# Optimization experiments

Measured on AMD Instinct MI355X. Metric: run time of the kernel, lower is better.

The kernel has to match this reference:

```python
import jax, jax.numpy as jnp
import numpy as np

N, F, H, C = 4096, 512, 8, 128
LEAKY_ALPHA = 0.2
MASK_VAL = -10e9  # spektral uses -10e9 * (1 - A)


def setup_inputs() -> dict:
    key = jax.random.key(0)
    k1, k2, k3, k4, k5 = jax.random.split(key, 5)
    X = jax.random.normal(k1, (N, F), dtype=jnp.float32)
    # sparse-ish binary adjacency with self loops (dense layout as the layer expects)
    A = (jax.random.uniform(k2, (N, N)) < 0.01).astype(jnp.float32)
    A = jnp.maximum(A, jnp.eye(N, dtype=jnp.float32))
    W = jax.random.normal(k3, (H, F, C), dtype=jnp.float32) * (1.0 / np.sqrt(F))
    a_self = jax.random.normal(k4, (H, C), dtype=jnp.float32) * (1.0 / np.sqrt(C))
    a_neigh = jax.random.normal(k5, (H, C), dtype=jnp.float32) * (1.0 / np.sqrt(C))
    bias = jnp.zeros((H, C), dtype=jnp.float32)
    return {"X": X, "A": A, "W": W, "a_self": a_self, "a_neigh": a_neigh, "bias": bias}


def reference(X, A, W, a_self, a_neigh, bias):
    # per-head feature projection: [H, N, C]
    feats = jnp.einsum("nf,hfc->hnc", X, W)
    # attention scores e_ij = LeakyReLU(a_self . h_i + a_neigh . h_j)
    s_self = jnp.einsum("hnc,hc->hn", feats, a_self)    # [H, N]
    s_neigh = jnp.einsum("hnc,hc->hn", feats, a_neigh)  # [H, N]
    dense = s_self[:, :, None] + s_neigh[:, None, :]    # [H, N, N]
    dense = jnp.where(dense > 0, dense, LEAKY_ALPHA * dense)
    # adjacency mask then row softmax (dropout_rate=0 -> identity)
    dense = dense + MASK_VAL * (1.0 - A)[None, :, :]
    coef = jax.nn.softmax(dense, axis=-1)               # [H, N, N]
    out = jnp.einsum("hnm,hmc->hnc", coef, feats)       # [H, N, C]
    out = out + bias[:, None, :]
    # concat heads: [N, H*C]
    out = jnp.transpose(out, (1, 0, 2)).reshape(N, H * C)
    return jax.nn.relu(out)
```

## Files before the change

kernel.cpp:

```cpp
#include <hip/hip_runtime.h>
#include <hip/hip_bf16.h>

#define GN 4096
#define GF 512
#define GH 8
#define GC 128
#define CAP 256
#define BK 64
#define XS 72

typedef __hip_bfloat16 bf16;
typedef unsigned short u16;
typedef unsigned int u32;
typedef __attribute__((ext_vector_type(8))) short bf16x8;
typedef __attribute__((ext_vector_type(4))) float f32x4;

static __device__ inline u16 f2u16(float x) {
    union { bf16 b; u16 u; } cv;
    cv.b = __float2bfloat16(x);
    return cv.u;
}

__global__ __launch_bounds__(256) void feats_kernel(
    const float* __restrict__ X, const float* __restrict__ W,
    const float* __restrict__ a_self, const float* __restrict__ a_neigh,
    bf16* __restrict__ featsb, float* __restrict__ s_self,
    float* __restrict__ s_neigh)
{
    __shared__ u16 sX[64 * XS];
    __shared__ u16 sW[128 * XS];

    int h   = blockIdx.x >> 6;
    int n0  = (blockIdx.x & 63) << 6;
    int tid = threadIdx.x;
    int lane = tid & 63, wv = tid >> 6;
    int lm = lane & 15, q = lane >> 4;

    const float* Xp = X + (size_t)n0 * GF;
    const float* Wh = W + (size_t)h * GF * GC;

    int xrow = tid >> 4, xq4 = tid & 15;
    int wk = tid >> 5, wn4 = tid & 31;

    float4 xr[4], wr[8];

#define ISSUE_TILE(K0)                                                        \
    {                                                                         \
        _Pragma("unroll")                                                     \
        for (int it = 0; it < 4; ++it)                                        \
            xr[it] = *(const float4*)&Xp[(size_t)(it * 16 + xrow) * GF +      \
                                         (K0) + xq4 * 4];                     \
        _Pragma("unroll")                                                     \
        for (int it = 0; it < 8; ++it)                                        \
            wr[it] = *(const float4*)&Wh[(size_t)((K0) + it * 8 + wk) * GC +  \
                                         wn4 * 4];                            \
    }

#define STORE_TILE()                                                          \
    {                                                                         \
        _Pragma("unroll")                                                     \
        for (int it = 0; it < 4; ++it) {                                      \
            u16* d = &sX[(it * 16 + xrow) * XS + xq4 * 4];                    \
            d[0] = f2u16(xr[it].x); d[1] = f2u16(xr[it].y);                   \
            d[2] = f2u16(xr[it].z); d[3] = f2u16(xr[it].w);                   \
        }                                                                     \
        _Pragma("unroll")                                                     \
        for (int it = 0; it < 8; ++it) {                                      \
            int k = it * 8 + wk;                                              \
            sW[(wn4 * 4 + 0) * XS + k] = f2u16(wr[it].x);                     \
            sW[(wn4 * 4 + 1) * XS + k] = f2u16(wr[it].y);                     \
            sW[(wn4 * 4 + 2) * XS + k] = f2u16(wr[it].z);                     \
            sW[(wn4 * 4 + 3) * XS + k] = f2u16(wr[it].w);                     \
        }                                                                     \
    }

    f32x4 acc[8];
#pragma unroll
    for (int nt = 0; nt < 8; ++nt) acc[nt] = (f32x4){0.f, 0.f, 0.f, 0.f};

    ISSUE_TILE(0)
    STORE_TILE()

    for (int k0 = 0; k0 < GF; k0 += BK) {
        __syncthreads();
        if (k0 + BK < GF) ISSUE_TILE(k0 + BK)

#pragma unroll
        for (int ks = 0; ks < BK; ks += 32) {
            bf16x8 af = *(const bf16x8*)&sX[(wv * 16 + lm) * XS + ks + q * 8];
            bf16x8 bfr[8];
#pragma unroll
            for (int nt = 0; nt < 8; ++nt)
                bfr[nt] = *(const bf16x8*)&sW[(nt * 16 + lm) * XS + ks + q * 8];
#pragma unroll
            for (int nt = 0; nt < 8; ++nt)
                acc[nt] = __builtin_amdgcn_mfma_f32_16x16x32_bf16(
                    af, bfr[nt], acc[nt], 0, 0, 0);
        }
        __syncthreads();
        if (k0 + BK < GF) STORE_TILE()
    }

    float aS[8], aN[8];
#pragma unroll
    for (int nt = 0; nt < 8; ++nt) {
        aS[nt] = a_self[h * GC + nt * 16 + lm];
        aN[nt] = a_neigh[h * GC + nt * 16 + lm];
    }
    float vs[4] = {0.f, 0.f, 0.f, 0.f};
    float vn[4] = {0.f, 0.f, 0.f, 0.f};
    int rbase = n0 + wv * 16 + q * 4;
#pragma unroll
    for (int nt = 0; nt < 8; ++nt) {
        f32x4 v = acc[nt];
        int col = nt * 16 + lm;
#pragma unroll
        for (int r = 0; r < 4; ++r) {
            featsb[((size_t)h * GN + rbase + r) * GC + col] = __float2bfloat16(v[r]);
            vs[r] += v[r] * aS[nt];
            vn[r] += v[r] * aN[nt];
        }
    }
#pragma unroll
    for (int r = 0; r < 4; ++r) {
        for (int off = 1; off < 16; off <<= 1) {
            vs[r] += __shfl_xor(vs[r], off);
            vn[r] += __shfl_xor(vn[r], off);
        }
        if (lm == 0) {
            s_self[h * GN + rbase + r]  = vs[r];
            s_neigh[h * GN + rbase + r] = vn[r];
        }
    }
#undef ISSUE_TILE
#undef STORE_TILE
}

__global__ __launch_bounds__(256) void csr_kernel(
    const float* __restrict__ A, int* __restrict__ deg,
    u16* __restrict__ lists)
{
    int i    = blockIdx.x;
    int tid  = threadIdx.x;
    int lane = tid & 63;
    __shared__ int cnt;
    if (tid == 0) cnt = 0;
    __syncthreads();

    u16* row = lists + (size_t)i * CAP;
    const float4* Arow = (const float4*)(A + (size_t)i * GN);
    unsigned long long ltmask = (lane == 63) ? ~0ull >> 1
                                             : (1ull << lane) - 1;
#pragma unroll
    for (int it = 0; it < 4; ++it) {
        int qd = it * 256 + tid;
        float4 a = Arow[qd];
        int j = qd * 4;
#pragma unroll
        for (int comp = 0; comp < 4; ++comp) {
            float av = comp == 0 ? a.x : comp == 1 ? a.y : comp == 2 ? a.z : a.w;
            bool flag = av > 0.5f;
            unsigned long long m = __ballot(flag);
            if (m) {
                int base = 0;
                if (lane == 0) base = atomicAdd(&cnt, __popcll(m));
                base = __shfl(base, 0);
                if (flag) {
                    int s = base + __popcll(m & ltmask);
                    if (s < CAP) row[s] = (u16)(j + comp);
                }
            }
        }
    }
    __syncthreads();
    if (tid == 0) deg[i] = cnt < CAP ? cnt : CAP;
}

__global__ __launch_bounds__(256) void attn_kernel(
    const int* __restrict__ deg, const u16* __restrict__ lists,
    const float* __restrict__ bias, const bf16* __restrict__ featsb,
    const float* __restrict__ s_self, const float* __restrict__ s_neigh,
    float* __restrict__ out)
{
    int tid  = threadIdx.x;
    int wv   = tid >> 6, lane = tid & 63;
    int g    = blockIdx.x * 4 + wv;
    int h    = g >> 12;
    int i    = g & (GN - 1);

    __shared__ float2 pjbuf[4][CAP];
    float2* pj = pjbuf[wv];

    int M = deg[i];
    const u16* row = lists + (size_t)i * CAP;
    float ssi = s_self[h * GN + i];
    const float* snh = s_neigh + h * GN;

    float lmax = -1e30f;
    for (int k = lane; k < M; k += 64) {
        int j = row[k];
        float e = ssi + snh[j];
        e = e > 0.f ? e : 0.2f * e;
        pj[k] = make_float2(e, __int_as_float(j));
        lmax = fmaxf(lmax, e);
    }
#pragma unroll
    for (int off = 32; off > 0; off >>= 1)
        lmax = fmaxf(lmax, __shfl_xor(lmax, off));

    float lsum = 0.f;
    for (int k = lane; k < M; k += 64) {
        float e = __expf(pj[k].x - lmax);
        pj[k].x = e;
        lsum += e;
    }
#pragma unroll
    for (int off = 32; off > 0; off >>= 1) lsum += __shfl_xor(lsum, off);
    float inv = 1.f / lsum;

    const u32* fh = (const u32*)(featsb + (size_t)h * GN * GC) + lane;
    float acc0 = 0.f, acc1 = 0.f;
#pragma unroll 4
    for (int k = 0; k < M; ++k) {
        float2 v = pj[k];
        int j = __float_as_int(v.y);
        u32 u = fh[(size_t)j << 6];
        acc0 += v.x * __uint_as_float(u << 16);
        acc1 += v.x * __uint_as_float(u & 0xffff0000u);
    }

    const float2 bv = *(const float2*)&bias[h * GC + 2 * lane];
    float r0 = acc0 * inv + bv.x;
    float r1 = acc1 * inv + bv.y;
    float2* op = (float2*)&out[(size_t)i * (GH * GC) + h * GC + 2 * lane];
    *op = make_float2(fmaxf(r0, 0.f), fmaxf(r1, 0.f));
}

extern "C" void kernel_launch(void* const* d_in, const int* in_sizes, int n_in,
                              void* d_out, int out_size, void* d_ws, size_t ws_size,
                              hipStream_t stream)
{
    const float* X       = (const float*)d_in[0];
    const float* A       = (const float*)d_in[1];
    const float* W       = (const float*)d_in[2];
    const float* a_self  = (const float*)d_in[3];
    const float* a_neigh = (const float*)d_in[4];
    const float* bias    = (const float*)d_in[5];
    float* out = (float*)d_out;

    bf16*  featsb  = (bf16*)d_ws;
    float* s_self  = (float*)(featsb + (size_t)GH * GN * GC);
    float* s_neigh = s_self + (size_t)GH * GN;
    int*   deg     = (int*)(s_neigh + (size_t)GH * GN);
    u16*   lists   = (u16*)(deg + GN);

    feats_kernel<<<GH * 64, 256, 0, stream>>>(X, W, a_self, a_neigh,
                                              featsb, s_self, s_neigh);
    csr_kernel<<<GN, 256, 0, stream>>>(A, deg, lists);
    attn_kernel<<<GH * GN / 4, 256, 0, stream>>>(deg, lists, bias, featsb,
                                                 s_self, s_neigh, out);
}
```

Measured before the change: 180.8 us.

## Pre-convert X and transposed W to bf16, load MFMA fragments directly from global

Adds a prep kernel that converts X to bf16 and writes W per head as a transposed bf16 [C,F] layout. The projection GEMM then drops its LDS staging and barriers and reads MFMA operand fragments straight from global memory, relying on L2 for reuse. This removes the fp32 loads, per-block conversions and shared-memory traffic from the GEMM, at the cost of an extra launch, extra workspace, and uncoalesced global fragment loads with no LDS reuse across waves.

```diff
diff --git a/kernel.cpp b/kernel.cpp
--- a/kernel.cpp
+++ b/kernel.cpp
@@ -6,8 +6,6 @@
 #define GH 8
 #define GC 128
 #define CAP 256
-#define BK 64
-#define XS 72
 
 typedef __hip_bfloat16 bf16;
 typedef unsigned short u16;
@@ -21,84 +19,73 @@
     return cv.u;
 }
 
+__global__ __launch_bounds__(256) void prep_kernel(
+    const float* __restrict__ X, const float* __restrict__ W,
+    u16* __restrict__ Xb, u16* __restrict__ WT)
+{
+    int tid = threadIdx.x;
+    if (blockIdx.x < 1024) {
+        size_t idx = ((size_t)blockIdx.x * 256 + tid) * 8;
+        float4 v0 = *(const float4*)(X + idx);
+        float4 v1 = *(const float4*)(X + idx + 4);
+        u16 o[8] = {f2u16(v0.x), f2u16(v0.y), f2u16(v0.z), f2u16(v0.w),
+                    f2u16(v1.x), f2u16(v1.y), f2u16(v1.z), f2u16(v1.w)};
+        *(bf16x8*)(Xb + idx) = *(bf16x8*)o;
+        return;
+    }
+    int wb = blockIdx.x - 1024;
+    int h  = wb >> 3;
+    int s16 = (wb & 7) * 16;
+    __shared__ u16 sT[16][520];
+
+    const float* Wh = W + (size_t)h * GF * GC;
+    for (int pass = 0; pass < 8; ++pass) {
+        int k  = pass * 64 + (tid >> 2);
+        int n4 = tid & 3;
+        float4 v = *(const float4*)&Wh[(size_t)k * GC + s16 + n4 * 4];
+        sT[n4 * 4 + 0][k] = f2u16(v.x);
+        sT[n4 * 4 + 1][k] = f2u16(v.y);
+        sT[n4 * 4 + 2][k] = f2u16(v.z);
+        sT[n4 * 4 + 3][k] = f2u16(v.w);
+    }
+    __syncthreads();
+    int n = tid >> 4, seg = tid & 15;
+    u16* dst = WT + ((size_t)h * GC + s16 + n) * GF + seg * 32;
+#pragma unroll
+    for (int s = 0; s < 4; ++s)
+        *(bf16x8*)(dst + s * 8) = *(const bf16x8*)&sT[n][seg * 32 + s * 8];
+}
+
 __global__ __launch_bounds__(256) void feats_kernel(
-    const float* __restrict__ X, const float* __restrict__ W,
+    const u16* __restrict__ Xb, const u16* __restrict__ WT,
     const float* __restrict__ a_self, const float* __restrict__ a_neigh,
     bf16* __restrict__ featsb, float* __restrict__ s_self,
     float* __restrict__ s_neigh)
 {
-    __shared__ u16 sX[64 * XS];
-    __shared__ u16 sW[128 * XS];
-
     int h   = blockIdx.x >> 6;
     int n0  = (blockIdx.x & 63) << 6;
     int tid = threadIdx.x;
     int lane = tid & 63, wv = tid >> 6;
     int lm = lane & 15, q = lane >> 4;
 
-    const float* Xp = X + (size_t)n0 * GF;
-    const float* Wh = W + (size_t)h * GF * GC;
-
-    int xrow = tid >> 4, xq4 = tid & 15;
-    int wk = tid >> 5, wn4 = tid & 31;
-
-    float4 xr[4], wr[8];
-
-#define ISSUE_TILE(K0)                                                        \
-    {                                                                         \
-        _Pragma("unroll")                                                     \
-        for (int it = 0; it < 4; ++it)                                        \
-            xr[it] = *(const float4*)&Xp[(size_t)(it * 16 + xrow) * GF +      \
-                                         (K0) + xq4 * 4];                     \
-        _Pragma("unroll")                                                     \
-        for (int it = 0; it < 8; ++it)                                        \
-            wr[it] = *(const float4*)&Wh[(size_t)((K0) + it * 8 + wk) * GC +  \
-                                         wn4 * 4];                            \
-    }
-
-#define STORE_TILE()                                                          \
-    {                                                                         \
-        _Pragma("unroll")                                                     \
-        for (int it = 0; it < 4; ++it) {                                      \
-            u16* d = &sX[(it * 16 + xrow) * XS + xq4 * 4];                    \
-            d[0] = f2u16(xr[it].x); d[1] = f2u16(xr[it].y);                   \
-            d[2] = f2u16(xr[it].z); d[3] = f2u16(xr[it].w);                   \
-        }                                                                     \
-        _Pragma("unroll")                                                     \
-        for (int it = 0; it < 8; ++it) {                                      \
-            int k = it * 8 + wk;                                              \
-            sW[(wn4 * 4 + 0) * XS + k] = f2u16(wr[it].x);                     \
-            sW[(wn4 * 4 + 1) * XS + k] = f2u16(wr[it].y);                     \
-            sW[(wn4 * 4 + 2) * XS + k] = f2u16(wr[it].z);                     \
-            sW[(wn4 * 4 + 3) * XS + k] = f2u16(wr[it].w);                     \
-        }                                                                     \
-    }
+    const u16* xrow = Xb + (size_t)(n0 + wv * 16 + lm) * GF + q * 8;
+    const u16* wrow = WT + (size_t)h * GC * GF + (size_t)lm * GF + q * 8;
 
     f32x4 acc[8];
 #pragma unroll
     for (int nt = 0; nt < 8; ++nt) acc[nt] = (f32x4){0.f, 0.f, 0.f, 0.f};
 
-    ISSUE_TILE(0)
-    STORE_TILE()
-
-    for (int k0 = 0; k0 < GF; k0 += BK) {
-        __syncthreads();
-        if (k0 + BK < GF) ISSUE_TILE(k0 + BK)
-
-#pragma unroll
-        for (int ks = 0; ks < BK; ks += 32) {
-            bf16x8 af = *(const bf16x8*)&sX[(wv * 16 + lm) * XS + ks + q * 8];
-            bf16x8 bfr[8];
-#pragma unroll
-            for (int nt = 0; nt < 8; ++nt)
-                bfr[nt] = *(const bf16x8*)&sW[(nt * 16 + lm) * XS + ks + q * 8];
-#pragma unroll
-            for (int nt = 0; nt < 8; ++nt)
-                acc[nt] = __builtin_amdgcn_mfma_f32_16x16x32_bf16(
-                    af, bfr[nt], acc[nt], 0, 0, 0);
-        }
-        __syncthreads();
-        if (k0 + BK < GF) STORE_TILE()
+#pragma unroll 2
+    for (int ks = 0; ks < GF; ks += 32) {
+        bf16x8 af = *(const bf16x8*)(xrow + ks);
+        bf16x8 bfr[8];
+#pragma unroll
+        for (int nt = 0; nt < 8; ++nt)
+            bfr[nt] = *(const bf16x8*)(wrow + (size_t)nt * 16 * GF + ks);
+#pragma unroll
+        for (int nt = 0; nt < 8; ++nt)
+            acc[nt] = __builtin_amdgcn_mfma_f32_16x16x32_bf16(
+                af, bfr[nt], acc[nt], 0, 0, 0);
     }
 
     float aS[8], aN[8];
@@ -132,8 +119,6 @@
             s_neigh[h * GN + rbase + r] = vn[r];
         }
     }
-#undef ISSUE_TILE
-#undef STORE_TILE
 }
 
 __global__ __launch_bounds__(256) void csr_kernel(
@@ -253,8 +238,11 @@
     float* s_neigh = s_self + (size_t)GH * GN;
     int*   deg     = (int*)(s_neigh + (size_t)GH * GN);
     u16*   lists   = (u16*)(deg + GN);
-
-    feats_kernel<<<GH * 64, 256, 0, stream>>>(X, W, a_self, a_neigh,
+    u16*   Xb      = lists + (size_t)GN * CAP;
+    u16*   WT      = Xb + (size_t)GN * GF;
+
+    prep_kernel<<<1088, 256, 0, stream>>>(X, W, Xb, WT);
+    feats_kernel<<<GH * 64, 256, 0, stream>>>(Xb, WT, a_self, a_neigh,
                                               featsb, s_self, s_neigh);
     csr_kernel<<<GN, 256, 0, stream>>>(A, deg, lists);
     attn_kernel<<<GH * GN / 4, 256, 0, stream>>>(deg, lists, bias, featsb,
```

After: 186.3 us. +3.0%, slower.
